# Performance work log

Measured on AMD Instinct MI355X. Metric: run time of the kernel, lower is better.

The kernel has to match this reference:

```python
import jax, jax.numpy as jnp
import numpy as np

B, T, C, R, S, SO, O, L = 4, 8192, 128, 64, 256, 256, 256, 16
LOOP = 9  # floor(log2(256)) + 1
DIL = [2 ** (i % LOOP) for i in range(L)]  # dilation schedule per layer
SQRT_HALF = float(np.sqrt(0.5))


def setup_inputs() -> dict:
    key = jax.random.key(0)
    ks = jax.random.split(key, 10)
    n = lambda k, shape, s=0.05: (jax.random.normal(k, shape) * s).astype(jnp.float32)
    return dict(
        features=jax.random.normal(ks[0], (B, C, T), dtype=jnp.float32),
        tokens=jax.random.randint(ks[1], (B, T), 0, 256),
        embed=n(ks[2], (256, R)),
        cond_W=n(ks[3], (2 * R * L, C)),
        cond_b=jnp.zeros((2 * R * L,), jnp.float32),
        dilate_W=n(ks[4], (L, 2 * R, R, 2)),
        dilate_b=jnp.zeros((L, 2 * R), jnp.float32),
        res_W=n(ks[5], (L - 1, R, R)),
        res_b=jnp.zeros((L - 1, R), jnp.float32),
        skip_W=n(ks[6], (L, S, R)),
        skip_b=jnp.zeros((L, S), jnp.float32),
        conv_out_W=n(ks[7], (SO, S)),
        conv_end_W=n(ks[8], (O, SO)),
    )


def wavenet_fwd(features, tokens, embed, cond_W, cond_b, dilate_W, dilate_b,
                res_W, res_b, skip_W, skip_b, conv_out_W, conv_end_W):
    # quantized input layer: embedding then (B, T, R) -> (B, R, T)
    x = embed[tokens].transpose(0, 2, 1)
    # 1x1 conditioning conv, reshaped to per-layer chunks [B, L, 2R, T]
    cond = (jnp.einsum('oc,bct->bot', cond_W, features)
            + cond_b[None, :, None]).reshape(B, L, 2 * R, T)
    in_acts = []
    skip_out = None
    res_acts = None
    for i in range(L):
        d = DIL[i]
        # causal dilated conv, kernel=2: out[t] = W0 @ x[t-d] + W1 @ x[t] + b
        x_prev = jnp.pad(x, ((0, 0), (0, 0), (d, 0)))[:, :, :T]
        ia = (jnp.einsum('oi,bit->bot', dilate_W[i, :, :, 0], x_prev)
              + jnp.einsum('oi,bit->bot', dilate_W[i, :, :, 1], x)
              + dilate_b[i][None, :, None])
        in_acts.append(ia)
        a = ia + cond[:, i]
        acts = jnp.tanh(a[:, :R]) * jax.nn.sigmoid(a[:, R:])  # gated activation
        if i < L - 1:
            res_acts = jnp.einsum('oi,bit->bot', res_W[i], acts) + res_b[i][None, :, None]
        # NOTE: last layer reuses the previous layer's res_acts (faithful to torch source)
        x = (res_acts + x) * SQRT_HALF
        skip = jnp.einsum('oi,bit->bot', skip_W[i], acts) + skip_b[i][None, :, None]
        skip_out = skip if i == 0 else skip_out + skip
    h = jax.nn.relu(skip_out)
    h = jax.nn.relu(jnp.einsum('oi,bit->bot', conv_out_W, h))
    out = jnp.einsum('oi,bit->bot', conv_end_W, h)
    # shift right by one: prepend a zero frame, drop the last
    out = jnp.concatenate([jnp.zeros_like(out[:, :, :1]), out[:, :, :-1]], axis=2)
    return out, (jnp.stack(in_acts, axis=1), cond)


def reference(features, tokens, embed, cond_W, cond_b, dilate_W, dilate_b,
              res_W, res_b, skip_W, skip_b, conv_out_W, conv_end_W):
    return wavenet_fwd(features, tokens, embed, cond_W, cond_b, dilate_W, dilate_b,
                       res_W, res_b, skip_W, skip_b, conv_out_W, conv_end_W)
```

## Files before the change

### kernel.cpp

```cpp
#include <hip/hip_runtime.h>
#include <cstdint>

namespace {
constexpr int B = 4, T = 8192, C = 128, R = 64, S = 256, SO = 256, O = 256, L = 16;
constexpr float SQRT_HALF = 0.70710678118654752440f;
}

__device__ __forceinline__ float fsigm(float x) { return 1.0f / (1.0f + __expf(-x)); }
__device__ __forceinline__ float ftanh(float x) { return 1.0f - 2.0f / (1.0f + __expf(2.0f * x)); }

__device__ __forceinline__ int uni(int v) { return __builtin_amdgcn_readfirstlane(v); }

__global__ __launch_bounds__(256) void k_embed(const int* __restrict__ tokens,
                                               const float* __restrict__ embed,
                                               float* __restrict__ x) {
  int blk = blockIdx.x;
  int b = blk >> 7;
  int t0 = (blk & 127) << 6;
  int lane = threadIdx.x & 63;
  int w = threadIdx.x >> 6;
  int t = t0 + lane;
  int tok = tokens[b * T + t];
  const float* e = embed + tok * R + w * 16;
  float* xp = x + ((size_t)b * R + w * 16) * T + t;
#pragma unroll
  for (int j = 0; j < 16; ++j) xp[(size_t)j * T] = e[j];
}

__global__ __launch_bounds__(256) void k_cond(const float* __restrict__ feat,
                                              const float* __restrict__ condW,
                                              const float* __restrict__ condb,
                                              float* __restrict__ cond_out) {
  int blk = blockIdx.x;
  int b = blk >> 7;
  int t0 = (blk & 127) << 6;
  int lane = threadIdx.x & 63;
  int w = threadIdx.x >> 6;
  int oc = blockIdx.y;
  int o0 = uni(oc * 256 + w * 64);
  int t = t0 + lane;
  float f[C];
  const float* fb = feat + (size_t)b * C * T + t;
#pragma unroll
  for (int k = 0; k < C; ++k) f[k] = fb[(size_t)k * T];
  float* outp = cond_out + ((size_t)b * (2 * R * L) + o0) * T + t;
  for (int j = 0; j < 64; ++j) {
    const float* wr = condW + (size_t)(o0 + j) * C;
    float acc = condb[o0 + j];
#pragma unroll
    for (int k = 0; k < C; ++k) acc = fmaf(wr[k], f[k], acc);
    outp[(size_t)j * T] = acc;
  }
}

__global__ __launch_bounds__(256) void k_layer(const float* __restrict__ x_in,
                                               float* __restrict__ x_out,
                                               const float* __restrict__ cond,
                                               const float* __restrict__ dW,
                                               const float* __restrict__ db,
                                               const float* __restrict__ resW,
                                               const float* __restrict__ resb,
                                               float* __restrict__ ia_out,
                                               int l, int d, int last) {
  __shared__ float acts[64][64];
  int blk = blockIdx.x;
  int b = blk >> 7;
  int t0 = (blk & 127) << 6;
  int lane = threadIdx.x & 63;
  int w = threadIdx.x >> 6;
  int t = t0 + lane;
  const float* xb = x_in + (size_t)b * R * T;
  float xc[R], xp[R];
#pragma unroll
  for (int k = 0; k < R; ++k) xc[k] = xb[(size_t)k * T + t];
  if (t >= d) {
#pragma unroll
    for (int k = 0; k < R; ++k) xp[k] = xb[(size_t)k * T + t - d];
  } else {
#pragma unroll
    for (int k = 0; k < R; ++k) xp[k] = 0.0f;
  }
  const float* cnd = cond + (size_t)(b * L + l) * 128 * T + t;
  float* iao = ia_out + (size_t)(b * L + l) * 128 * T + t;
  int p0 = uni(w * 16);
  for (int p = p0; p < p0 + 16; ++p) {
    const float* w1 = dW + (size_t)p * 128;
    const float* w2 = dW + (size_t)(p + 64) * 128;
    float a1 = db[p], a2 = db[p + 64];
#pragma unroll
    for (int k = 0; k < R; ++k) {
      a1 = fmaf(w1[2 * k], xp[k], a1);
      a1 = fmaf(w1[2 * k + 1], xc[k], a1);
      a2 = fmaf(w2[2 * k], xp[k], a2);
      a2 = fmaf(w2[2 * k + 1], xc[k], a2);
    }
    iao[(size_t)p * T] = a1;
    iao[(size_t)(p + 64) * T] = a2;
    a1 += cnd[(size_t)p * T];
    a2 += cnd[(size_t)(p + 64) * T];
    acts[p][lane] = ftanh(a1) * fsigm(a2);
  }
  __syncthreads();
  if (!last) {
    float areg[R];
#pragma unroll
    for (int k = 0; k < R; ++k) areg[k] = acts[k][lane];
    float* xo = x_out + (size_t)b * R * T + t;
    for (int o = p0; o < p0 + 16; ++o) {
      const float* wr = resW + (size_t)o * R;
      float acc = resb[o];
#pragma unroll
      for (int k = 0; k < R; ++k) acc = fmaf(wr[k], areg[k], acc);
      xo[(size_t)o * T] = (acc + xb[(size_t)o * T + t]) * SQRT_HALF;
    }
  }
}

__global__ __launch_bounds__(256) void k_skip(const float* __restrict__ ia,
                                              const float* __restrict__ cond,
                                              const float* __restrict__ skipW,
                                              const float* __restrict__ skipb,
                                              float* __restrict__ skip_out) {
  int blk = blockIdx.x;
  int b = blk >> 7;
  int t0 = (blk & 127) << 6;
  int lane = threadIdx.x & 63;
  int w = threadIdx.x >> 6;
  int t = t0 + lane;
  int s0 = uni(w * 64);
  float acc[64];
#pragma unroll
  for (int j = 0; j < 64; ++j) {
    float bs = 0.0f;
    for (int l = 0; l < L; ++l) bs += skipb[l * S + s0 + j];
    acc[j] = bs;
  }
  for (int l = 0; l < L; ++l) {
    const float* iab = ia + (size_t)(b * L + l) * 128 * T + t;
    const float* cnb = cond + (size_t)(b * L + l) * 128 * T + t;
    float areg[R];
#pragma unroll
    for (int k = 0; k < R; ++k) {
      float a1 = iab[(size_t)k * T] + cnb[(size_t)k * T];
      float a2 = iab[(size_t)(k + 64) * T] + cnb[(size_t)(k + 64) * T];
      areg[k] = ftanh(a1) * fsigm(a2);
    }
    const float* sw = skipW + (size_t)l * S * R + (size_t)s0 * R;
#pragma unroll
    for (int j = 0; j < 64; ++j) {
      const float* wr = sw + (size_t)j * R;
      float a = acc[j];
#pragma unroll
      for (int k = 0; k < R; ++k) a = fmaf(wr[k], areg[k], a);
      acc[j] = a;
    }
  }
  float* sp = skip_out + ((size_t)b * S + s0) * T + t;
#pragma unroll
  for (int j = 0; j < 64; ++j) sp[(size_t)j * T] = acc[j];
}

__global__ __launch_bounds__(256) void k_head(const float* __restrict__ skip_in,
                                              const float* __restrict__ Wout,
                                              const float* __restrict__ Wend,
                                              float* __restrict__ out) {
  __shared__ float hbuf[SO][64];
  int blk = blockIdx.x;
  int b = blk >> 7;
  int t0 = (blk & 127) << 6;
  int lane = threadIdx.x & 63;
  int w = threadIdx.x >> 6;
  int t = t0 + lane;
  int g0 = uni(w * 64);
  float acc[64];
#pragma unroll
  for (int j = 0; j < 64; ++j) acc[j] = 0.0f;
  for (int c = 0; c < 4; ++c) {
    float areg[64];
    const float* sp = skip_in + ((size_t)b * S + c * 64) * T + t;
#pragma unroll
    for (int k = 0; k < 64; ++k) areg[k] = fmaxf(sp[(size_t)k * T], 0.0f);
#pragma unroll
    for (int j = 0; j < 64; ++j) {
      const float* wr = Wout + (size_t)(g0 + j) * S + c * 64;
      float a = acc[j];
#pragma unroll
      for (int k = 0; k < 64; ++k) a = fmaf(wr[k], areg[k], a);
      acc[j] = a;
    }
  }
#pragma unroll
  for (int j = 0; j < 64; ++j) hbuf[g0 + j][lane] = fmaxf(acc[j], 0.0f);
  __syncthreads();
#pragma unroll
  for (int j = 0; j < 64; ++j) acc[j] = 0.0f;
  for (int c = 0; c < 4; ++c) {
    float areg[64];
#pragma unroll
    for (int k = 0; k < 64; ++k) areg[k] = hbuf[c * 64 + k][lane];
#pragma unroll
    for (int j = 0; j < 64; ++j) {
      const float* wr = Wend + (size_t)(g0 + j) * SO + c * 64;
      float a = acc[j];
#pragma unroll
      for (int k = 0; k < 64; ++k) a = fmaf(wr[k], areg[k], a);
      acc[j] = a;
    }
  }
  float* ob = out + ((size_t)b * O + g0) * T;
  if (t + 1 < T) {
#pragma unroll
    for (int j = 0; j < 64; ++j) ob[(size_t)j * T + t + 1] = acc[j];
  }
  if (t0 == 0 && lane == 0) {
#pragma unroll
    for (int j = 0; j < 64; ++j) ob[(size_t)j * T] = 0.0f;
  }
}

extern "C" void kernel_launch(void* const* d_in, const int* in_sizes, int n_in,
                              void* d_out, int out_size, void* d_ws, size_t ws_size,
                              hipStream_t stream) {
  const float* features   = (const float*)d_in[0];
  const int*   tokens     = (const int*)d_in[1];
  const float* embed      = (const float*)d_in[2];
  const float* cond_W     = (const float*)d_in[3];
  const float* cond_b     = (const float*)d_in[4];
  const float* dilate_W   = (const float*)d_in[5];
  const float* dilate_b   = (const float*)d_in[6];
  const float* res_W      = (const float*)d_in[7];
  const float* res_b      = (const float*)d_in[8];
  const float* skip_W     = (const float*)d_in[9];
  const float* skip_b     = (const float*)d_in[10];
  const float* conv_out_W = (const float*)d_in[11];
  const float* conv_end_W = (const float*)d_in[12];

  float* out  = (float*)d_out;
  float* ia   = out + (size_t)B * O * T;
  float* cond = ia + (size_t)B * L * 2 * R * T;

  float* xa   = (float*)d_ws;
  float* xb   = xa + (size_t)B * R * T;
  float* skip = xb + (size_t)B * R * T;

  dim3 blk(256);
  int nblk = B * (T / 64);

  k_embed<<<nblk, blk, 0, stream>>>(tokens, embed, xa);
  k_cond<<<dim3(nblk, 8), blk, 0, stream>>>(features, cond_W, cond_b, cond);

  static const int DIL[L] = {1, 2, 4, 8, 16, 32, 64, 128, 256, 1, 2, 4, 8, 16, 32, 64};
  float* xcur = xa;
  float* xnxt = xb;
  for (int l = 0; l < L; ++l) {
    int lr = (l < L - 1) ? l : 0;
    k_layer<<<nblk, blk, 0, stream>>>(xcur, xnxt, cond,
                                      dilate_W + (size_t)l * 128 * 64 * 2,
                                      dilate_b + (size_t)l * 128,
                                      res_W + (size_t)lr * 64 * 64,
                                      res_b + (size_t)lr * 64,
                                      ia, l, DIL[l], (l == L - 1) ? 1 : 0);
    float* tmp = xcur; xcur = xnxt; xnxt = tmp;
  }
  k_skip<<<nblk, blk, 0, stream>>>(ia, cond, skip_W, skip_b, skip);
  k_head<<<nblk, blk, 0, stream>>>(skip, conv_out_W, conv_end_W, out);
}
```

Baseline: 5.112 ms.

## Stage activations in LDS once per block and tile channel reductions by 16

Each kernel now loads its input channels from global memory once per block, with each wave loading a disjoint slice into shared memory. Reductions then run over 16-channel chunks read from LDS, instead of every wave redundantly loading all channels into registers. The skip kernel also double-buffers the next layer's in_acts and cond loads into registers and LDS while the current layer's matmul runs. This removes four-fold redundant global loads and lowers register pressure, at the cost of more LDS use and extra barriers that may reduce occupancy.

Result: slower. 6.525 ms (+27.7%).

```diff
diff --git a/kernel.cpp b/kernel.cpp
--- a/kernel.cpp
+++ b/kernel.cpp
@@ -31,6 +31,7 @@
                                               const float* __restrict__ condW,
                                               const float* __restrict__ condb,
                                               float* __restrict__ cond_out) {
+  __shared__ float fs[C][64];
   int blk = blockIdx.x;
   int b = blk >> 7;
   int t0 = (blk & 127) << 6;
@@ -38,19 +39,31 @@
   int w = threadIdx.x >> 6;
   int oc = blockIdx.y;
   int o0 = uni(oc * 256 + w * 64);
-  int t = t0 + lane;
-  float f[C];
+  int cs = uni(w * 32);
+  int t = t0 + lane;
   const float* fb = feat + (size_t)b * C * T + t;
 #pragma unroll
-  for (int k = 0; k < C; ++k) f[k] = fb[(size_t)k * T];
+  for (int j = 0; j < 32; ++j) fs[cs + j][lane] = fb[(size_t)(cs + j) * T];
+  __syncthreads();
+  float acc[64];
+#pragma unroll
+  for (int j = 0; j < 64; ++j) acc[j] = condb[o0 + j];
+  for (int kc = 0; kc < 8; ++kc) {
+    float areg[16];
+#pragma unroll
+    for (int k = 0; k < 16; ++k) areg[k] = fs[kc * 16 + k][lane];
+#pragma unroll
+    for (int j = 0; j < 64; ++j) {
+      const float* wr = condW + (size_t)(o0 + j) * C + kc * 16;
+      float a = acc[j];
+#pragma unroll
+      for (int k = 0; k < 16; ++k) a = fmaf(wr[k], areg[k], a);
+      acc[j] = a;
+    }
+  }
   float* outp = cond_out + ((size_t)b * (2 * R * L) + o0) * T + t;
-  for (int j = 0; j < 64; ++j) {
-    const float* wr = condW + (size_t)(o0 + j) * C;
-    float acc = condb[o0 + j];
-#pragma unroll
-    for (int k = 0; k < C; ++k) acc = fmaf(wr[k], f[k], acc);
-    outp[(size_t)j * T] = acc;
-  }
+#pragma unroll
+  for (int j = 0; j < 64; ++j) outp[(size_t)j * T] = acc[j];
 }
 
 __global__ __launch_bounds__(256) void k_layer(const float* __restrict__ x_in,
@@ -62,6 +75,8 @@
                                                const float* __restrict__ resb,
                                                float* __restrict__ ia_out,
                                                int l, int d, int last) {
+  __shared__ float xs[64][64];
+  __shared__ float xps[64][64];
   __shared__ float acts[64][64];
   int blk = blockIdx.x;
   int b = blk >> 7;
@@ -69,49 +84,83 @@
   int lane = threadIdx.x & 63;
   int w = threadIdx.x >> 6;
   int t = t0 + lane;
+  int p0 = uni(w * 16);
   const float* xb = x_in + (size_t)b * R * T;
-  float xc[R], xp[R];
-#pragma unroll
-  for (int k = 0; k < R; ++k) xc[k] = xb[(size_t)k * T + t];
-  if (t >= d) {
-#pragma unroll
-    for (int k = 0; k < R; ++k) xp[k] = xb[(size_t)k * T + t - d];
-  } else {
-#pragma unroll
-    for (int k = 0; k < R; ++k) xp[k] = 0.0f;
-  }
   const float* cnd = cond + (size_t)(b * L + l) * 128 * T + t;
+  float c1[16], c2[16];
+#pragma unroll
+  for (int j = 0; j < 16; ++j) {
+    c1[j] = cnd[(size_t)(p0 + j) * T];
+    c2[j] = cnd[(size_t)(p0 + j + 64) * T];
+  }
+#pragma unroll
+  for (int j = 0; j < 16; ++j) {
+    int ch = p0 + j;
+    xs[ch][lane] = xb[(size_t)ch * T + t];
+    xps[ch][lane] = (t >= d) ? xb[(size_t)ch * T + t - d] : 0.0f;
+  }
+  __syncthreads();
+  float a1[16], a2[16];
+#pragma unroll
+  for (int j = 0; j < 16; ++j) { a1[j] = db[p0 + j]; a2[j] = db[p0 + j + 64]; }
+#pragma unroll
+  for (int kc = 0; kc < 4; ++kc) {
+    float xcr[16], xpr[16];
+#pragma unroll
+    for (int k = 0; k < 16; ++k) {
+      xcr[k] = xs[kc * 16 + k][lane];
+      xpr[k] = xps[kc * 16 + k][lane];
+    }
+#pragma unroll
+    for (int j = 0; j < 16; ++j) {
+      const float* w1 = dW + (size_t)(p0 + j) * 128 + kc * 32;
+      const float* w2 = dW + (size_t)(p0 + j + 64) * 128 + kc * 32;
+      float s1 = a1[j], s2 = a2[j];
+#pragma unroll
+      for (int k = 0; k < 16; ++k) {
+        s1 = fmaf(w1[2 * k], xpr[k], s1);
+        s1 = fmaf(w1[2 * k + 1], xcr[k], s1);
+        s2 = fmaf(w2[2 * k], xpr[k], s2);
+        s2 = fmaf(w2[2 * k + 1], xcr[k], s2);
+      }
+      a1[j] = s1; a2[j] = s2;
+    }
+  }
   float* iao = ia_out + (size_t)(b * L + l) * 128 * T + t;
-  int p0 = uni(w * 16);
-  for (int p = p0; p < p0 + 16; ++p) {
-    const float* w1 = dW + (size_t)p * 128;
-    const float* w2 = dW + (size_t)(p + 64) * 128;
-    float a1 = db[p], a2 = db[p + 64];
-#pragma unroll
-    for (int k = 0; k < R; ++k) {
-      a1 = fmaf(w1[2 * k], xp[k], a1);
-      a1 = fmaf(w1[2 * k + 1], xc[k], a1);
-      a2 = fmaf(w2[2 * k], xp[k], a2);
-      a2 = fmaf(w2[2 * k + 1], xc[k], a2);
-    }
-    iao[(size_t)p * T] = a1;
-    iao[(size_t)(p + 64) * T] = a2;
-    a1 += cnd[(size_t)p * T];
-    a2 += cnd[(size_t)(p + 64) * T];
-    acts[p][lane] = ftanh(a1) * fsigm(a2);
+#pragma unroll
+  for (int j = 0; j < 16; ++j) {
+    iao[(size_t)(p0 + j) * T] = a1[j];
+    iao[(size_t)(p0 + j + 64) * T] = a2[j];
+  }
+#pragma unroll
+  for (int j = 0; j < 16; ++j) {
+    float g1 = a1[j] + c1[j];
+    float g2 = a2[j] + c2[j];
+    acts[p0 + j][lane] = ftanh(g1) * fsigm(g2);
   }
   __syncthreads();
   if (!last) {
-    float areg[R];
-#pragma unroll
-    for (int k = 0; k < R; ++k) areg[k] = acts[k][lane];
+    float racc[16];
+#pragma unroll
+    for (int j = 0; j < 16; ++j) racc[j] = resb[p0 + j];
+#pragma unroll
+    for (int kc = 0; kc < 4; ++kc) {
+      float areg[16];
+#pragma unroll
+      for (int k = 0; k < 16; ++k) areg[k] = acts[kc * 16 + k][lane];
+#pragma unroll
+      for (int j = 0; j < 16; ++j) {
+        const float* wr = resW + (size_t)(p0 + j) * R + kc * 16;
+        float a = racc[j];
+#pragma unroll
+        for (int k = 0; k < 16; ++k) a = fmaf(wr[k], areg[k], a);
+        racc[j] = a;
+      }
+    }
     float* xo = x_out + (size_t)b * R * T + t;
-    for (int o = p0; o < p0 + 16; ++o) {
-      const float* wr = resW + (size_t)o * R;
-      float acc = resb[o];
-#pragma unroll
-      for (int k = 0; k < R; ++k) acc = fmaf(wr[k], areg[k], acc);
-      xo[(size_t)o * T] = (acc + xb[(size_t)o * T + t]) * SQRT_HALF;
+#pragma unroll
+    for (int j = 0; j < 16; ++j) {
+      xo[(size_t)(p0 + j) * T] = (racc[j] + xs[p0 + j][lane]) * SQRT_HALF;
     }
   }
 }
@@ -121,6 +170,8 @@
                                               const float* __restrict__ skipW,
                                               const float* __restrict__ skipb,
                                               float* __restrict__ skip_out) {
+  __shared__ float raw[2][128][64];
+  __shared__ float acts[64][64];
   int blk = blockIdx.x;
   int b = blk >> 7;
   int t0 = (blk & 127) << 6;
@@ -128,6 +179,9 @@
   int w = threadIdx.x >> 6;
   int t = t0 + lane;
   int s0 = uni(w * 64);
+  int kg = uni(w * 16);
+  int cs = uni(w * 32);
+
   float acc[64];
 #pragma unroll
   for (int j = 0; j < 64; ++j) {
@@ -135,24 +189,61 @@
     for (int l = 0; l < L; ++l) bs += skipb[l * S + s0 + j];
     acc[j] = bs;
   }
+
+  const float* iab0 = ia + (size_t)(b * L) * 128 * T + t;
+  const float* cnb0 = cond + (size_t)(b * L) * 128 * T + t;
+
+  float sreg[32], c1[16], c2[16];
+#pragma unroll
+  for (int j = 0; j < 32; ++j) sreg[j] = iab0[(size_t)(cs + j) * T];
+#pragma unroll
+  for (int j = 0; j < 16; ++j) {
+    c1[j] = cnb0[(size_t)(kg + j) * T];
+    c2[j] = cnb0[(size_t)(kg + j + 64) * T];
+  }
+#pragma unroll
+  for (int j = 0; j < 32; ++j) raw[0][cs + j][lane] = sreg[j];
+
+  int cur = 0;
   for (int l = 0; l < L; ++l) {
-    const float* iab = ia + (size_t)(b * L + l) * 128 * T + t;
-    const float* cnb = cond + (size_t)(b * L + l) * 128 * T + t;
-    float areg[R];
-#pragma unroll
-    for (int k = 0; k < R; ++k) {
-      float a1 = iab[(size_t)k * T] + cnb[(size_t)k * T];
-      float a2 = iab[(size_t)(k + 64) * T] + cnb[(size_t)(k + 64) * T];
-      areg[k] = ftanh(a1) * fsigm(a2);
+    __syncthreads();
+#pragma unroll
+    for (int j = 0; j < 16; ++j) {
+      float g1 = raw[cur][kg + j][lane] + c1[j];
+      float g2 = raw[cur][kg + j + 64][lane] + c2[j];
+      acts[kg + j][lane] = ftanh(g1) * fsigm(g2);
+    }
+    __syncthreads();
+    if (l + 1 < L) {
+      const float* iab = iab0 + (size_t)(l + 1) * 128 * T;
+      const float* cnb = cnb0 + (size_t)(l + 1) * 128 * T;
+#pragma unroll
+      for (int j = 0; j < 32; ++j) sreg[j] = iab[(size_t)(cs + j) * T];
+#pragma unroll
+      for (int j = 0; j < 16; ++j) {
+        c1[j] = cnb[(size_t)(kg + j) * T];
+        c2[j] = cnb[(size_t)(kg + j + 64) * T];
+      }
     }
     const float* sw = skipW + (size_t)l * S * R + (size_t)s0 * R;
 #pragma unroll
-    for (int j = 0; j < 64; ++j) {
-      const float* wr = sw + (size_t)j * R;
-      float a = acc[j];
-#pragma unroll
-      for (int k = 0; k < R; ++k) a = fmaf(wr[k], areg[k], a);
-      acc[j] = a;
+    for (int kc = 0; kc < 4; ++kc) {
+      float areg[16];
+#pragma unroll
+      for (int k = 0; k < 16; ++k) areg[k] = acts[kc * 16 + k][lane];
+#pragma unroll
+      for (int j = 0; j < 64; ++j) {
+        const float* wr = sw + (size_t)j * R + kc * 16;
+        float a = acc[j];
+#pragma unroll
+        for (int k = 0; k < 16; ++k) a = fmaf(wr[k], areg[k], a);
+        acc[j] = a;
+      }
+    }
+    if (l + 1 < L) {
+#pragma unroll
+      for (int j = 0; j < 32; ++j) raw[cur ^ 1][cs + j][lane] = sreg[j];
+      cur ^= 1;
     }
   }
   float* sp = skip_out + ((size_t)b * S + s0) * T + t;
@@ -164,7 +255,7 @@
                                               const float* __restrict__ Wout,
                                               const float* __restrict__ Wend,
                                               float* __restrict__ out) {
-  __shared__ float hbuf[SO][64];
+  __shared__ float ss[SO][64];
   int blk = blockIdx.x;
   int b = blk >> 7;
   int t0 = (blk & 127) << 6;
@@ -172,38 +263,43 @@
   int w = threadIdx.x >> 6;
   int t = t0 + lane;
   int g0 = uni(w * 64);
+  const float* sp = skip_in + (size_t)b * S * T + t;
+#pragma unroll
+  for (int j = 0; j < 64; ++j)
+    ss[g0 + j][lane] = fmaxf(sp[(size_t)(g0 + j) * T], 0.0f);
+  __syncthreads();
   float acc[64];
 #pragma unroll
   for (int j = 0; j < 64; ++j) acc[j] = 0.0f;
-  for (int c = 0; c < 4; ++c) {
-    float areg[64];
-    const float* sp = skip_in + ((size_t)b * S + c * 64) * T + t;
-#pragma unroll
-    for (int k = 0; k < 64; ++k) areg[k] = fmaxf(sp[(size_t)k * T], 0.0f);
+  for (int kc = 0; kc < 16; ++kc) {
+    float areg[16];
+#pragma unroll
+    for (int k = 0; k < 16; ++k) areg[k] = ss[kc * 16 + k][lane];
 #pragma unroll
     for (int j = 0; j < 64; ++j) {
-      const float* wr = Wout + (size_t)(g0 + j) * S + c * 64;
+      const float* wr = Wout + (size_t)(g0 + j) * S + kc * 16;
       float a = acc[j];
 #pragma unroll
-      for (int k = 0; k < 64; ++k) a = fmaf(wr[k], areg[k], a);
+      for (int k = 0; k < 16; ++k) a = fmaf(wr[k], areg[k], a);
       acc[j] = a;
     }
   }
-#pragma unroll
-  for (int j = 0; j < 64; ++j) hbuf[g0 + j][lane] = fmaxf(acc[j], 0.0f);
+  __syncthreads();
+#pragma unroll
+  for (int j = 0; j < 64; ++j) ss[g0 + j][lane] = fmaxf(acc[j], 0.0f);
   __syncthreads();
 #pragma unroll
   for (int j = 0; j < 64; ++j) acc[j] = 0.0f;
-  for (int c = 0; c < 4; ++c) {
-    float areg[64];
-#pragma unroll
-    for (int k = 0; k < 64; ++k) areg[k] = hbuf[c * 64 + k][lane];
+  for (int kc = 0; kc < 16; ++kc) {
+    float areg[16];
+#pragma unroll
+    for (int k = 0; k < 16; ++k) areg[k] = ss[kc * 16 + k][lane];
 #pragma unroll
     for (int j = 0; j < 64; ++j) {
-      const float* wr = Wend + (size_t)(g0 + j) * SO + c * 64;
+      const float* wr = Wend + (size_t)(g0 + j) * SO + kc * 16;
       float a = acc[j];
 #pragma unroll
-      for (int k = 0; k < 64; ++k) a = fmaf(wr[k], areg[k], a);
+      for (int k = 0; k < 16; ++k) a = fmaf(wr[k], areg[k], a);
       acc[j] = a;
     }
   }
```
